# Optimization experiments

Measured on AMD Instinct MI355X. Metric: run time of the kernel, lower is better.

Reference implementation:

```python
import jax, jax.numpy as jnp
import numpy as np

D_MODEL = 1024
N_HEADS = 16
DEPTH = D_MODEL // N_HEADS
DFF = 4096
B, S = 2, 2048
EPS = 1e-6


def layer_norm(x, gamma, beta):
    m = jnp.mean(x, axis=-1, keepdims=True)
    v = jnp.mean(jnp.square(x - m), axis=-1, keepdims=True)
    return (x - m) * jax.lax.rsqrt(v + EPS) * gamma + beta


def setup_inputs() -> dict:
    key = jax.random.key(0)
    ks = jax.random.split(key, 16)
    s = 0.02
    x = jax.random.normal(ks[0], (B, S, D_MODEL), dtype=jnp.float32)
    # causal mask: 1.0 where attention is NOT allowed (upper triangle)
    mask = (1.0 - jnp.tril(jnp.ones((S, S), dtype=jnp.float32)))[None, None, :, :]
    return {
        "x": x,
        "mask": mask,
        "wq": jax.random.normal(ks[1], (D_MODEL, D_MODEL), jnp.float32) * s,
        "bq": jnp.zeros((D_MODEL,), jnp.float32),
        "wk": jax.random.normal(ks[2], (D_MODEL, D_MODEL), jnp.float32) * s,
        "bk": jnp.zeros((D_MODEL,), jnp.float32),
        "wv": jax.random.normal(ks[3], (D_MODEL, D_MODEL), jnp.float32) * s,
        "bv": jnp.zeros((D_MODEL,), jnp.float32),
        "wo": jax.random.normal(ks[4], (D_MODEL, D_MODEL), jnp.float32) * s,
        "bo": jnp.zeros((D_MODEL,), jnp.float32),
        "g1": jnp.ones((D_MODEL,), jnp.float32),
        "be1": jnp.zeros((D_MODEL,), jnp.float32),
        "w1": jax.random.normal(ks[5], (D_MODEL, DFF), jnp.float32) * s,
        "b1": jnp.zeros((DFF,), jnp.float32),
        "w2": jax.random.normal(ks[6], (DFF, D_MODEL), jnp.float32) * s,
        "b2": jnp.zeros((D_MODEL,), jnp.float32),
        "g2": jnp.ones((D_MODEL,), jnp.float32),
        "be2": jnp.zeros((D_MODEL,), jnp.float32),
    }


def reference(x, mask, wq, bq, wk, bk, wv, bv, wo, bo, g1, be1, w1, b1, w2, b2, g2, be2):
    b, s = x.shape[0], x.shape[1]

    def heads(t):  # [B,S,D_MODEL] -> [B,H,S,depth]
        return t.reshape(b, s, N_HEADS, DEPTH).transpose(0, 2, 1, 3)

    q = heads(x @ wq + bq)
    k = heads(x @ wk + bk)
    v = heads(x @ wv + bv)

    # [B,H,S,S] scores, materialized as in the original
    logits = jnp.einsum("bhqd,bhkd->bhqk", q, k) / jnp.sqrt(jnp.float32(DEPTH))
    logits = logits + mask * (-1e9)
    attn = jax.nn.softmax(logits, axis=-1)
    ctx = jnp.einsum("bhqk,bhkd->bhqd", attn, v)
    ctx = ctx.transpose(0, 2, 1, 3).reshape(b, s, D_MODEL)
    attn_out = ctx @ wo + bo

    out1 = layer_norm(x + attn_out, g1, be1)
    ffn = jax.nn.relu(out1 @ w1 + b1) @ w2 + b2
    out2 = layer_norm(out1 + ffn, g2, be2)
    return out2  # dropout inactive (training=False)
```

## Files before the change

### kernel.cpp

```cpp
#include <hip/hip_runtime.h>
#include <stdint.h>

typedef unsigned short u16;
typedef unsigned int u32;
typedef __attribute__((ext_vector_type(8))) short short8;
typedef __attribute__((ext_vector_type(4))) float f32x4;

#define NHEADS 16
#define SEQ 2048
#define DM 1024
#define MROWS 4096
#define FF 4096

static_assert(sizeof(short8) == 16, "short8 must be 16B");

__device__ __forceinline__ u16 f2b(float f) {
  u32 u = __float_as_uint(f);
  u += 0x7fffu + ((u >> 16) & 1u);
  return (u16)(u >> 16);
}
__device__ __forceinline__ u32 f2b2(float lo, float hi) {
  u32 a = __float_as_uint(lo); a += 0x7fffu + ((a >> 16) & 1u);
  u32 b = __float_as_uint(hi); b += 0x7fffu + ((b >> 16) & 1u);
  return (a >> 16) | (b & 0xffff0000u);
}
__device__ __forceinline__ u32 f2b2t(float lo, float hi) {
  return __builtin_amdgcn_perm(__float_as_uint(hi), __float_as_uint(lo), 0x07060302u);
}
__device__ __forceinline__ float b2f(u16 h) { return __uint_as_float(((u32)h) << 16); }

__device__ __forceinline__ void async_cp16(const u16* g, u16* l) {
  __builtin_amdgcn_global_load_lds((const __attribute__((address_space(1))) void*)g,
                                   (__attribute__((address_space(3))) void*)l, 16, 0, 0);
}

__global__ __launch_bounds__(256) void prep_k(const float* __restrict__ x,
                                              const float* __restrict__ wq,
                                              const float* __restrict__ wk,
                                              const float* __restrict__ wv,
                                              const float* __restrict__ wo,
                                              const float* __restrict__ w1,
                                              const float* __restrict__ w2,
                                              u16* __restrict__ xb, u16* __restrict__ btq,
                                              u16* __restrict__ wot, u16* __restrict__ w1t,
                                              u16* __restrict__ w2t) {
  const int bid = blockIdx.x, tid = threadIdx.x;
  if (bid < 4096) {
    const int i = bid * 256 + tid;
    const float4 v = ((const float4*)x)[i];
    uint2 o; o.x = f2b2(v.x, v.y); o.y = f2b2(v.z, v.w);
    ((uint2*)xb)[i] = o;
    return;
  }
  __shared__ float tile[32][33];
  const int tb = bid - 4096;
  const float* in; u16* out; int N, K, n0, k0;
  if (tb < 4096) {
    const int m = tb >> 10, t = tb & 1023;
    if (m == 0) { in = wq; out = btq; }
    else if (m == 1) { in = wk; out = btq + 1024 * 1024; }
    else if (m == 2) { in = wv; out = btq + 2 * 1024 * 1024; }
    else { in = wo; out = wot; }
    N = 1024; K = 1024; n0 = (t & 31) * 32; k0 = (t >> 5) * 32;
  } else if (tb < 8192) {
    const int t = tb - 4096;
    in = w1; out = w1t; N = 4096; K = 1024; n0 = (t & 127) * 32; k0 = (t >> 7) * 32;
  } else {
    const int t = tb - 8192;
    in = w2; out = w2t; N = 1024; K = 4096; n0 = (t & 31) * 32; k0 = (t >> 5) * 32;
  }
  const int tx = tid & 31, ty = tid >> 5;
#pragma unroll
  for (int i = 0; i < 4; i++) {
    const int r = ty + i * 8;
    tile[r][tx] = in[(long)(k0 + r) * N + n0 + tx];
  }
  __syncthreads();
#pragma unroll
  for (int i = 0; i < 4; i++) {
    const int r = ty + i * 8;
    out[(long)(n0 + r) * K + k0 + tx] = f2b(tile[tx][r]);
  }
}

#define BM 128
#define BN 128
#define BK 64
#define EPI_QKV 0
#define EPI_RELUB 2
#define EPI_PART 3

template <int EPI>
__global__ __launch_bounds__(256, 2) void gemm_bt(
    const u16* __restrict__ A, const u16* __restrict__ Bt, const int M, const int N,
    const int KITER, const int LDA, const int KOFF,
    const float* __restrict__ bias0, const float* __restrict__ bias1,
    const float* __restrict__ bias2,
    float* __restrict__ outF, u16* __restrict__ outB, u16* __restrict__ outQ,
    u16* __restrict__ outK, u16* __restrict__ outV) {
  __shared__ u16 As[BM * BK];
  __shared__ u16 Bs[BN * BK];
  const int tid = threadIdx.x;
  const int lane = tid & 63;
  const int wv = tid >> 6;
  const int quad = lane >> 4;
  const int lm = lane & 15;
  const int lid = blockIdx.y * gridDim.x + blockIdx.x;
  const int s = lid >> 3;
  const int tm = ((lid & 7) * 4 + (s & 3)) * BM;
  const int tn = (s >> 2) * BN;
  const int wr = (wv >> 1) * 64;
  const int wc = (wv & 1) * 64;
  const int wslotbase = tid & ~63;
  const long zoff = (long)blockIdx.z * KOFF;
  const u16* Ap = A + zoff;
  const u16* Btp = Bt + zoff;

  const f32x4 z4 = {0.f, 0.f, 0.f, 0.f};
  f32x4 acc[4][4];
#pragma unroll
  for (int i = 0; i < 4; i++)
#pragma unroll
    for (int j = 0; j < 4; j++) acc[i][j] = z4;

  for (int kk = 0; kk < KITER; kk += BK) {
    __syncthreads();
#pragma unroll
    for (int t = 0; t < 4; t++) {
      const int slot = t * 256 + tid;
      const int row = slot >> 3;
      const int c = (slot & 7) ^ (row & 7);
      async_cp16(Ap + (long)(tm + row) * LDA + kk + c * 8,
                 As + (long)(t * 256 + wslotbase) * 8);
    }
#pragma unroll
    for (int t = 0; t < 4; t++) {
      const int slot = t * 256 + tid;
      const int row = slot >> 3;
      const int c = (slot & 7) ^ (row & 7);
      async_cp16(Btp + (long)(tn + row) * LDA + kk + c * 8,
                 Bs + (long)(t * 256 + wslotbase) * 8);
    }
    __syncthreads();
#pragma unroll
    for (int ks = 0; ks < 2; ks++) {
      short8 af[4], bf[4];
#pragma unroll
      for (int mi = 0; mi < 4; mi++) {
        const int row = wr + mi * 16 + lm;
        const int cc = (4 * ks + quad) ^ (row & 7);
        af[mi] = *(const short8*)(As + row * 64 + cc * 8);
      }
#pragma unroll
      for (int ni = 0; ni < 4; ni++) {
        const int row = wc + ni * 16 + lm;
        const int cc = (4 * ks + quad) ^ (row & 7);
        bf[ni] = *(const short8*)(Bs + row * 64 + cc * 8);
      }
#pragma unroll
      for (int mi = 0; mi < 4; mi++)
#pragma unroll
        for (int ni = 0; ni < 4; ni++)
          acc[mi][ni] =
              __builtin_amdgcn_mfma_f32_16x16x32_bf16(af[mi], bf[ni], acc[mi][ni], 0, 0, 0);
    }
  }

  if constexpr (EPI == EPI_QKV) {
    const int which = tn >> 10;
    const int bb = tm >> 11;
    if (which < 2) {
      const float* bs = which == 0 ? bias0 : bias1;
      u16* os = which == 0 ? outQ : outK;
      const float scale = which == 0 ? 0.125f * 1.44269504f : 1.0f;
#pragma unroll
      for (int ni = 0; ni < 4; ni++) {
        const int n = tn + wc + ni * 16 + lm;
        const int hd = n & 1023;
        const int h = hd >> 6, dep = hd & 63;
        const float bval = bs[hd];
#pragma unroll
        for (int mi = 0; mi < 4; mi++) {
#pragma unroll
          for (int r = 0; r < 4; r++) {
            const int ss = (tm & 2047) + wr + mi * 16 + quad * 4 + r;
            os[(((long)(bb * NHEADS + h) * SEQ + ss) << 6) + dep] =
                f2b((acc[mi][ni][r] + bval) * scale);
          }
        }
      }
    } else {
#pragma unroll
      for (int ni = 0; ni < 4; ni++) {
        const int n = tn + wc + ni * 16 + lm;
        const int hd = n & 1023;
        const int h = hd >> 6, dep = hd & 63;
        const float bval = bias2[hd];
        u16* vrow = outV + ((long)(bb * NHEADS + h) * 64 + dep) * SEQ;
#pragma unroll
        for (int mi = 0; mi < 4; mi++) {
          const int ss = (tm & 2047) + wr + mi * 16 + quad * 4;
          uint2 o;
          o.x = f2b2(acc[mi][ni][0] + bval, acc[mi][ni][1] + bval);
          o.y = f2b2(acc[mi][ni][2] + bval, acc[mi][ni][3] + bval);
          *(uint2*)(vrow + ss) = o;
        }
      }
    }
  } else if constexpr (EPI == EPI_PART) {
    float* po = outF + (long)blockIdx.z * M * N;
#pragma unroll
    for (int mi = 0; mi < 4; mi++) {
#pragma unroll
      for (int r = 0; r < 4; r++) {
        const int m = tm + wr + mi * 16 + quad * 4 + r;
        const long rowo = (long)m * N;
#pragma unroll
        for (int ni = 0; ni < 4; ni++) {
          const int n = tn + wc + ni * 16 + lm;
          po[rowo + n] = acc[mi][ni][r];
        }
      }
    }
  } else {
#pragma unroll
    for (int mi = 0; mi < 4; mi++) {
#pragma unroll
      for (int r = 0; r < 4; r++) {
        const int m = tm + wr + mi * 16 + quad * 4 + r;
        const long rowo = (long)m * N;
#pragma unroll
        for (int ni = 0; ni < 4; ni++) {
          const int n = tn + wc + ni * 16 + lm;
          const float v = acc[mi][ni][r] + bias0[n];
          outB[rowo + n] = f2b(fmaxf(v, 0.f));
        }
      }
    }
  }
}

__global__ __launch_bounds__(256, 3) void attn_fused(const u16* __restrict__ Q,
                                                     const u16* __restrict__ K,
                                                     const u16* __restrict__ Vt,
                                                     u16* __restrict__ O,
                                                     float* __restrict__ part,
                                                     float* __restrict__ lpart) {
  __shared__ u16 Ks[2][64 * 64];
  __shared__ u16 Vs[2][64 * 64];
  __shared__ u16 Ps[4][16 * 72];
  const int tid = threadIdx.x;
  const int lane = tid & 63, w = tid >> 6, quad = lane >> 4, lm = lane & 15;
  const int bid = blockIdx.x;
  const int idx = bid >> 5, hb = bid & 31;
  const int h = hb & 15, b = hb >> 4;
  int qt, c0, nkl, half;
  if (idx < 32) {
    qt = 16 + (idx >> 1);
    const int nk = qt + 1;
    const int h0 = (nk + 1) >> 1;
    half = idx & 1;
    if (half == 0) { c0 = 0; nkl = h0; } else { c0 = h0; nkl = nk - h0; }
  } else {
    qt = 47 - idx; c0 = 0; nkl = qt + 1; half = -1;
  }
  const long bh = (long)(b * NHEADS + h);
  const u16* Qb = Q + bh * SEQ * 64;
  const u16* Kb = K + bh * SEQ * 64;
  const u16* Vb = Vt + bh * (long)64 * SEQ;
  const int rbase = qt * 64 + w * 16;
  const int wslot = tid & ~63;

  long kgo[2], vgo[2];
  int ldso[2];
#pragma unroll
  for (int i = 0; i < 2; i++) {
    const int slot = i * 256 + tid;
    const int row = slot >> 3;
    const int cg = (slot & 7) ^ (row & 7);
    kgo[i] = (long)row * 64 + cg * 8;
    vgo[i] = (long)row * SEQ + cg * 8;
    ldso[i] = (i * 256 + wslot) * 8;
  }

  short8 qf[2];
#pragma unroll
  for (int ks = 0; ks < 2; ks++)
    qf[ks] = *(const short8*)(Qb + (long)(rbase + lm) * 64 + ks * 32 + quad * 8);

  const f32x4 z4 = {0.f, 0.f, 0.f, 0.f};
  f32x4 ctx[4];
#pragma unroll
  for (int d = 0; d < 4; d++) ctx[d] = z4;
  float lacc = 0.f;
  u16* myP = (u16*)Ps[w];

  {
    const long ko = (long)c0 * 64 * 64;
#pragma unroll
    for (int i = 0; i < 2; i++) {
      async_cp16(Kb + ko + kgo[i], Ks[0] + ldso[i]);
      async_cp16(Vb + c0 * 64 + vgo[i], Vs[0] + ldso[i]);
    }
  }

  for (int t = 0; t < nkl; t++) {
    const int cur = t & 1;
    const int k0 = (c0 + t) * 64;
    __syncthreads();
    if (t + 1 < nkl) {
      const long ko = (long)(k0 + 64) * 64;
#pragma unroll
      for (int i = 0; i < 2; i++) {
        async_cp16(Kb + ko + kgo[i], Ks[1 - cur] + ldso[i]);
        async_cp16(Vb + (k0 + 64) + vgo[i], Vs[1 - cur] + ldso[i]);
      }
    }
    const u16* Kc = Ks[cur];
    const u16* Vc = Vs[cur];
    short8 kf[4][2];
#pragma unroll
    for (int ni = 0; ni < 4; ni++) {
      const int row = ni * 16 + lm;
      const int r8 = row & 7;
#pragma unroll
      for (int ks = 0; ks < 2; ks++) {
        const int cc = (ks * 4 + quad) ^ r8;
        kf[ni][ks] = *(const short8*)(Kc + row * 64 + cc * 8);
      }
    }
    f32x4 sa[4];
#pragma unroll
    for (int i = 0; i < 4; i++) sa[i] = z4;
#pragma unroll
    for (int ks = 0; ks < 2; ks++)
#pragma unroll
      for (int ni = 0; ni < 4; ni++)
        sa[ni] = __builtin_amdgcn_mfma_f32_16x16x32_bf16(kf[ni][ks], qf[ks], sa[ni], 0, 0, 0);
    const int qrow = rbase + lm;
    if (k0 + 63 > rbase) {
#pragma unroll
      for (int ni = 0; ni < 4; ni++)
#pragma unroll
        for (int r = 0; r < 4; r++)
          if (k0 + ni * 16 + quad * 4 + r > qrow) sa[ni][r] = -1e9f;
    }
    float tsum = 0.f;
#pragma unroll
    for (int ni = 0; ni < 4; ni++) {
      const float p0 = exp2f(sa[ni][0]);
      const float p1 = exp2f(sa[ni][1]);
      const float p2 = exp2f(sa[ni][2]);
      const float p3 = exp2f(sa[ni][3]);
      tsum += (p0 + p1) + (p2 + p3);
      uint2 o; o.x = f2b2t(p0, p1); o.y = f2b2t(p2, p3);
      *(uint2*)(myP + lm * 72 + ni * 16 + quad * 4) = o;
    }
    lacc += tsum;
#pragma unroll
    for (int kc = 0; kc < 2; kc++) {
      const short8 bp = *(const short8*)(myP + lm * 72 + kc * 32 + quad * 8);
#pragma unroll
      for (int dni = 0; dni < 4; dni++) {
        const int row = dni * 16 + lm;
        const int cc = (kc * 4 + quad) ^ (row & 7);
        const short8 vfr = *(const short8*)(Vc + row * 64 + cc * 8);
        ctx[dni] = __builtin_amdgcn_mfma_f32_16x16x32_bf16(vfr, bp, ctx[dni], 0, 0, 0);
      }
    }
  }
  float l = lacc;
  l += __shfl_xor(l, 16);
  l += __shfl_xor(l, 32);
  if (half < 0) {
    const float inv = 1.0f / l;
    const int s = rbase + lm;
    const long base = (long)(b * SEQ + s) * DM + h * 64;
#pragma unroll
    for (int dni = 0; dni < 4; dni++) {
      uint2 o;
      o.x = f2b2(ctx[dni][0] * inv, ctx[dni][1] * inv);
      o.y = f2b2(ctx[dni][2] * inv, ctx[dni][3] * inv);
      *(uint2*)(O + base + dni * 16 + quad * 4) = o;
    }
  } else {
    const long pt = ((long)(hb * 16 + (qt - 16))) * 2 + half;
    float* po = part + pt * 4096 + (w * 16 + lm) * 64;
#pragma unroll
    for (int dni = 0; dni < 4; dni++)
      *(float4*)(po + dni * 16 + quad * 4) =
          make_float4(ctx[dni][0], ctx[dni][1], ctx[dni][2], ctx[dni][3]);
    if (quad == 0) lpart[pt * 64 + w * 16 + lm] = l;
  }
}

__global__ __launch_bounds__(256) void attn_combine(const float* __restrict__ part,
                                                    const float* __restrict__ lpart,
                                                    u16* __restrict__ O) {
  const int g = blockIdx.x;
  const int hb = g >> 4, qtr = g & 15;
  const int h = hb & 15, b = hb >> 4;
  const int qt = 16 + qtr;
  const long pt0 = ((long)(hb * 16 + qtr)) * 2;
  const float* p0 = part + pt0 * 4096;
  const float* p1 = p0 + 4096;
  const float* lp = lpart + pt0 * 64;
  const int tid = threadIdx.x;
  const int row = tid >> 2, d0 = (tid & 3) * 16;
  const float inv = 1.0f / (lp[row] + lp[64 + row]);
  const long off = (long)(b * SEQ + qt * 64 + row) * DM + h * 64 + d0;
  u32 o[8];
#pragma unroll
  for (int i = 0; i < 4; i++) {
    const float4 a = *(const float4*)(p0 + row * 64 + d0 + i * 4);
    const float4 c = *(const float4*)(p1 + row * 64 + d0 + i * 4);
    o[i * 2 + 0] = f2b2((a.x + c.x) * inv, (a.y + c.y) * inv);
    o[i * 2 + 1] = f2b2((a.z + c.z) * inv, (a.w + c.w) * inv);
  }
  *(uint4*)(O + off) = make_uint4(o[0], o[1], o[2], o[3]);
  *(uint4*)(O + off + 8) = make_uint4(o[4], o[5], o[6], o[7]);
}

template <bool WB>
__global__ __launch_bounds__(256) void layernorm2_k(const float* __restrict__ p0,
                                                    const float* __restrict__ p1,
                                                    const float* __restrict__ resid,
                                                    const float* __restrict__ bias,
                                                    const float* __restrict__ gam,
                                                    const float* __restrict__ bet,
                                                    float* __restrict__ outF,
                                                    u16* __restrict__ outB) {
  __shared__ float red[8];
  const int row = blockIdx.x, tid = threadIdx.x;
  const long off = (long)row * DM;
  const float4 a4 = ((const float4*)(p0 + off))[tid];
  const float4 b4v = ((const float4*)(p1 + off))[tid];
  const float4 r4 = ((const float4*)(resid + off))[tid];
  const float4 bi4 = ((const float4*)bias)[tid];
  float4 v;
  v.x = a4.x + b4v.x + r4.x + bi4.x;
  v.y = a4.y + b4v.y + r4.y + bi4.y;
  v.z = a4.z + b4v.z + r4.z + bi4.z;
  v.w = a4.w + b4v.w + r4.w + bi4.w;
  float s1 = v.x + v.y + v.z + v.w;
  float s2 = v.x * v.x + v.y * v.y + v.z * v.z + v.w * v.w;
  s1 += __shfl_xor(s1, 1); s2 += __shfl_xor(s2, 1);
  s1 += __shfl_xor(s1, 2); s2 += __shfl_xor(s2, 2);
  s1 += __shfl_xor(s1, 4); s2 += __shfl_xor(s2, 4);
  s1 += __shfl_xor(s1, 8); s2 += __shfl_xor(s2, 8);
  s1 += __shfl_xor(s1, 16); s2 += __shfl_xor(s2, 16);
  s1 += __shfl_xor(s1, 32); s2 += __shfl_xor(s2, 32);
  if ((tid & 63) == 0) { red[tid >> 6] = s1; red[4 + (tid >> 6)] = s2; }
  __syncthreads();
  const float mean = (red[0] + red[1] + red[2] + red[3]) * (1.f / DM);
  const float ex2 = (red[4] + red[5] + red[6] + red[7]) * (1.f / DM);
  const float var = fmaxf(ex2 - mean * mean, 0.f);
  const float rs = rsqrtf(var + 1e-6f);
  const float4 g4 = ((const float4*)gam)[tid];
  const float4 be4 = ((const float4*)bet)[tid];
  const float o0 = (v.x - mean) * rs * g4.x + be4.x;
  const float o1 = (v.y - mean) * rs * g4.y + be4.y;
  const float o2 = (v.z - mean) * rs * g4.z + be4.z;
  const float o3 = (v.w - mean) * rs * g4.w + be4.w;
  ((float4*)(outF + off))[tid] = make_float4(o0, o1, o2, o3);
  if constexpr (WB) {
    uint2 o; o.x = f2b2(o0, o1); o.y = f2b2(o2, o3);
    ((uint2*)(outB + off))[tid] = o;
  }
}

extern "C" void kernel_launch(void* const* d_in, const int* in_sizes, int n_in,
                              void* d_out, int out_size, void* d_ws, size_t ws_size,
                              hipStream_t stream) {
  (void)in_sizes; (void)n_in; (void)out_size; (void)ws_size;
  const float* x = (const float*)d_in[0];
  const float* wq = (const float*)d_in[2];
  const float* bq = (const float*)d_in[3];
  const float* wk = (const float*)d_in[4];
  const float* bk = (const float*)d_in[5];
  const float* wv = (const float*)d_in[6];
  const float* bv = (const float*)d_in[7];
  const float* wo = (const float*)d_in[8];
  const float* bo = (const float*)d_in[9];
  const float* g1 = (const float*)d_in[10];
  const float* be1 = (const float*)d_in[11];
  const float* w1 = (const float*)d_in[12];
  const float* b1 = (const float*)d_in[13];
  const float* w2 = (const float*)d_in[14];
  const float* b2 = (const float*)d_in[15];
  const float* g2 = (const float*)d_in[16];
  const float* be2 = (const float*)d_in[17];
  float* out = (float*)d_out;
  uint8_t* ws = (uint8_t*)d_ws;
  const size_t MB = 1024ull * 1024ull;
  u16* wot = (u16*)(ws + 0 * MB);
  u16* w1t = (u16*)(ws + 2 * MB);
  u16* w2t = (u16*)(ws + 10 * MB);
  u16* btq = (u16*)(ws + 18 * MB);
  u16* xb  = (u16*)(ws + 24 * MB);
  u16* qb  = (u16*)(ws + 32 * MB);
  u16* kb  = (u16*)(ws + 40 * MB);
  u16* vt  = (u16*)(ws + 48 * MB);
  u16* ctxb = (u16*)(ws + 56 * MB);
  float* apart = (float*)(ws + 64 * MB);
  float* lpart = (float*)(ws + 81 * MB);
  float* part = (float*)(ws + 64 * MB);
  u16* o1b = (u16*)(ws + 96 * MB);
  float* o1f = (float*)(ws + 104 * MB);
  u16* h1 = (u16*)(ws + 18 * MB);

  prep_k<<<dim3(16384), dim3(256), 0, stream>>>(x, wq, wk, wv, wo, w1, w2, xb, btq, wot,
                                                w1t, w2t);

  gemm_bt<EPI_QKV><<<dim3(24, 32), dim3(256), 0, stream>>>(
      xb, btq, MROWS, 3072, 1024, 1024, 0, bq, bk, bv, nullptr, nullptr, qb, kb, vt);

  attn_fused<<<dim3(1536), dim3(256), 0, stream>>>(qb, kb, vt, ctxb, apart, lpart);
  attn_combine<<<dim3(512), dim3(256), 0, stream>>>(apart, lpart, ctxb);

  gemm_bt<EPI_PART><<<dim3(8, 32, 2), dim3(256), 0, stream>>>(
      ctxb, wot, MROWS, 1024, 512, 1024, 512, nullptr, nullptr, nullptr, part, nullptr,
      nullptr, nullptr, nullptr);

  layernorm2_k<true><<<dim3(4096), dim3(256), 0, stream>>>(
      part, part + (long)MROWS * DM, x, bo, g1, be1, o1f, o1b);

  gemm_bt<EPI_RELUB><<<dim3(32, 32), dim3(256), 0, stream>>>(
      o1b, w1t, MROWS, 4096, 1024, 1024, 0, b1, nullptr, nullptr, nullptr, h1, nullptr,
      nullptr, nullptr);

  gemm_bt<EPI_PART><<<dim3(8, 32, 2), dim3(256), 0, stream>>>(
      h1, w2t, MROWS, 1024, 2048, 4096, 2048, nullptr, nullptr, nullptr, part, nullptr,
      nullptr, nullptr, nullptr);

  layernorm2_k<false><<<dim3(4096), dim3(256), 0, stream>>>(
      part, part + (long)MROWS * DM, o1f, b2, g2, be2, out, nullptr);
}
```

Measured before the change: 346.8 us.

## Split causal attention into fixed 8-tile KV chunks with uniform partial combine

Replaces the half-split of long query tiles with a uniform scheme where every query tile is split into chunks of at most 8 KV tiles. Each block writes fp32 partial context and row sums, and a generalized combine kernel sums 1 to 4 partials per tile. Warps also skip fully masked KV tiles, and the workspace layout is reshuffled so the larger partial buffers fit. This is meant to balance work across blocks and raise the block count, at the cost of more partial writes and a heavier combine pass for every tile.

```diff
diff --git a/kernel.cpp b/kernel.cpp
--- a/kernel.cpp
+++ b/kernel.cpp
@@ -32,6 +32,19 @@
 __device__ __forceinline__ void async_cp16(const u16* g, u16* l) {
   __builtin_amdgcn_global_load_lds((const __attribute__((address_space(1))) void*)g,
                                    (__attribute__((address_space(3))) void*)l, 16, 0, 0);
+}
+
+__device__ __forceinline__ void decode_slot(int rslot, int& qt, int& chunk) {
+  if (rslot < 32) { qt = 31 - (rslot >> 2); chunk = rslot & 3; }
+  else if (rslot < 56) { const int r = rslot - 32; const int q = r / 3; qt = 23 - q; chunk = r - q * 3; }
+  else if (rslot < 72) { const int r = rslot - 56; qt = 15 - (r >> 1); chunk = r & 1; }
+  else { qt = 79 - rslot; chunk = 0; }
+}
+__device__ __forceinline__ void qt_slots(int qt, int& base, int& nch) {
+  if (qt >= 24) { base = (31 - qt) * 4; nch = 4; }
+  else if (qt >= 16) { base = 32 + (23 - qt) * 3; nch = 3; }
+  else if (qt >= 8) { base = 56 + (15 - qt) * 2; nch = 2; }
+  else { base = 72 + (7 - qt); nch = 1; }
 }
 
 __global__ __launch_bounds__(256) void prep_k(const float* __restrict__ x,
@@ -243,7 +256,6 @@
 __global__ __launch_bounds__(256, 3) void attn_fused(const u16* __restrict__ Q,
                                                      const u16* __restrict__ K,
                                                      const u16* __restrict__ Vt,
-                                                     u16* __restrict__ O,
                                                      float* __restrict__ part,
                                                      float* __restrict__ lpart) {
   __shared__ u16 Ks[2][64 * 64];
@@ -252,18 +264,12 @@
   const int tid = threadIdx.x;
   const int lane = tid & 63, w = tid >> 6, quad = lane >> 4, lm = lane & 15;
   const int bid = blockIdx.x;
-  const int idx = bid >> 5, hb = bid & 31;
+  const int rslot = bid >> 5, hb = bid & 31;
   const int h = hb & 15, b = hb >> 4;
-  int qt, c0, nkl, half;
-  if (idx < 32) {
-    qt = 16 + (idx >> 1);
-    const int nk = qt + 1;
-    const int h0 = (nk + 1) >> 1;
-    half = idx & 1;
-    if (half == 0) { c0 = 0; nkl = h0; } else { c0 = h0; nkl = nk - h0; }
-  } else {
-    qt = 47 - idx; c0 = 0; nkl = qt + 1; half = -1;
-  }
+  int qt, chunk;
+  decode_slot(rslot, qt, chunk);
+  const int c0 = chunk * 8;
+  const int nkl = min(8, qt + 1 - c0);
   const long bh = (long)(b * NHEADS + h);
   const u16* Qb = Q + bh * SEQ * 64;
   const u16* Kb = K + bh * SEQ * 64;
@@ -316,6 +322,7 @@
         async_cp16(Vb + (k0 + 64) + vgo[i], Vs[1 - cur] + ldso[i]);
       }
     }
+    if (k0 >= rbase + 16) continue;
     const u16* Kc = Ks[cur];
     const u16* Vc = Vs[cur];
     short8 kf[4][2];
@@ -372,51 +379,46 @@
   float l = lacc;
   l += __shfl_xor(l, 16);
   l += __shfl_xor(l, 32);
-  if (half < 0) {
-    const float inv = 1.0f / l;
-    const int s = rbase + lm;
-    const long base = (long)(b * SEQ + s) * DM + h * 64;
-#pragma unroll
-    for (int dni = 0; dni < 4; dni++) {
-      uint2 o;
-      o.x = f2b2(ctx[dni][0] * inv, ctx[dni][1] * inv);
-      o.y = f2b2(ctx[dni][2] * inv, ctx[dni][3] * inv);
-      *(uint2*)(O + base + dni * 16 + quad * 4) = o;
-    }
-  } else {
-    const long pt = ((long)(hb * 16 + (qt - 16))) * 2 + half;
-    float* po = part + pt * 4096 + (w * 16 + lm) * 64;
-#pragma unroll
-    for (int dni = 0; dni < 4; dni++)
-      *(float4*)(po + dni * 16 + quad * 4) =
-          make_float4(ctx[dni][0], ctx[dni][1], ctx[dni][2], ctx[dni][3]);
-    if (quad == 0) lpart[pt * 64 + w * 16 + lm] = l;
-  }
+  const long pt = (long)hb * 80 + rslot;
+  float* po = part + pt * 4096 + (w * 16 + lm) * 64;
+#pragma unroll
+  for (int dni = 0; dni < 4; dni++)
+    *(float4*)(po + dni * 16 + quad * 4) =
+        make_float4(ctx[dni][0], ctx[dni][1], ctx[dni][2], ctx[dni][3]);
+  if (quad == 0) lpart[pt * 64 + w * 16 + lm] = l;
 }
 
 __global__ __launch_bounds__(256) void attn_combine(const float* __restrict__ part,
                                                     const float* __restrict__ lpart,
                                                     u16* __restrict__ O) {
   const int g = blockIdx.x;
-  const int hb = g >> 4, qtr = g & 15;
+  const int hb = g & 31, qt = g >> 5;
   const int h = hb & 15, b = hb >> 4;
-  const int qt = 16 + qtr;
-  const long pt0 = ((long)(hb * 16 + qtr)) * 2;
-  const float* p0 = part + pt0 * 4096;
-  const float* p1 = p0 + 4096;
-  const float* lp = lpart + pt0 * 64;
+  int base, nch;
+  qt_slots(qt, base, nch);
+  const long pt0 = (long)hb * 80 + base;
   const int tid = threadIdx.x;
   const int row = tid >> 2, d0 = (tid & 3) * 16;
-  const float inv = 1.0f / (lp[row] + lp[64 + row]);
+  float lsum = 0.f;
+  float acc[16];
+#pragma unroll
+  for (int i = 0; i < 16; i++) acc[i] = 0.f;
+  for (int c = 0; c < nch; c++) {
+    lsum += lpart[(pt0 + c) * 64 + row];
+    const float* pp = part + (pt0 + c) * 4096 + row * 64 + d0;
+#pragma unroll
+    for (int i = 0; i < 4; i++) {
+      const float4 a = *(const float4*)(pp + i * 4);
+      acc[i * 4 + 0] += a.x; acc[i * 4 + 1] += a.y;
+      acc[i * 4 + 2] += a.z; acc[i * 4 + 3] += a.w;
+    }
+  }
+  const float inv = 1.0f / lsum;
   const long off = (long)(b * SEQ + qt * 64 + row) * DM + h * 64 + d0;
   u32 o[8];
 #pragma unroll
-  for (int i = 0; i < 4; i++) {
-    const float4 a = *(const float4*)(p0 + row * 64 + d0 + i * 4);
-    const float4 c = *(const float4*)(p1 + row * 64 + d0 + i * 4);
-    o[i * 2 + 0] = f2b2((a.x + c.x) * inv, (a.y + c.y) * inv);
-    o[i * 2 + 1] = f2b2((a.z + c.z) * inv, (a.w + c.w) * inv);
-  }
+  for (int i = 0; i < 8; i++)
+    o[i] = f2b2(acc[i * 2] * inv, acc[i * 2 + 1] * inv);
   *(uint4*)(O + off) = make_uint4(o[0], o[1], o[2], o[3]);
   *(uint4*)(O + off + 8) = make_uint4(o[4], o[5], o[6], o[7]);
 }
@@ -503,11 +505,12 @@
   u16* vt  = (u16*)(ws + 48 * MB);
   u16* ctxb = (u16*)(ws + 56 * MB);
   float* apart = (float*)(ws + 64 * MB);
-  float* lpart = (float*)(ws + 81 * MB);
+  float* lpart = (float*)(ws + 106 * MB);
   float* part = (float*)(ws + 64 * MB);
-  u16* o1b = (u16*)(ws + 96 * MB);
-  float* o1f = (float*)(ws + 104 * MB);
-  u16* h1 = (u16*)(ws + 18 * MB);
+  u16* o1b = (u16*)(ws + 32 * MB);
+  float* o1f = (float*)(ws + 40 * MB);
+  u16* h1 = (u16*)(ws + 64 * MB);
+  float* part2 = (float*)(ws + 96 * MB);
 
   prep_k<<<dim3(16384), dim3(256), 0, stream>>>(x, wq, wk, wv, wo, w1, w2, xb, btq, wot,
                                                 w1t, w2t);
@@ -515,8 +518,8 @@
   gemm_bt<EPI_QKV><<<dim3(24, 32), dim3(256), 0, stream>>>(
       xb, btq, MROWS, 3072, 1024, 1024, 0, bq, bk, bv, nullptr, nullptr, qb, kb, vt);
 
-  attn_fused<<<dim3(1536), dim3(256), 0, stream>>>(qb, kb, vt, ctxb, apart, lpart);
-  attn_combine<<<dim3(512), dim3(256), 0, stream>>>(apart, lpart, ctxb);
+  attn_fused<<<dim3(2560), dim3(256), 0, stream>>>(qb, kb, vt, apart, lpart);
+  attn_combine<<<dim3(1024), dim3(256), 0, stream>>>(apart, lpart, ctxb);
 
   gemm_bt<EPI_PART><<<dim3(8, 32, 2), dim3(256), 0, stream>>>(
       ctxb, wot, MROWS, 1024, 512, 1024, 512, nullptr, nullptr, nullptr, part, nullptr,
@@ -530,9 +533,9 @@
       nullptr, nullptr);
 
   gemm_bt<EPI_PART><<<dim3(8, 32, 2), dim3(256), 0, stream>>>(
-      h1, w2t, MROWS, 1024, 2048, 4096, 2048, nullptr, nullptr, nullptr, part, nullptr,
+      h1, w2t, MROWS, 1024, 2048, 4096, 2048, nullptr, nullptr, nullptr, part2, nullptr,
       nullptr, nullptr, nullptr);
 
   layernorm2_k<false><<<dim3(4096), dim3(256), 0, stream>>>(
-      part, part + (long)MROWS * DM, o1f, b2, g2, be2, out, nullptr);
-}
+      part2, part2 + (long)MROWS * DM, o1f, b2, g2, be2, out, nullptr);
+}
```

New measurement: 349.1 us. Within noise of the previous version (+0.7%).
